# Kernel optimization log

Measured on AMD Instinct MI355X. Metric: run time of the kernel, lower is better.

Reference implementation:

```python
import jax, jax.numpy as jnp
import numpy as np

DECAY = 0.9


def setup_inputs() -> dict:
    key = jax.random.key(0)
    ks = jax.random.split(key, 8)
    B, L, d_model = 4, 2048, 1024
    d_state = 16
    d_inner = 2 * d_model  # expand=2
    x = jax.random.normal(ks[0], (B, L, d_model), dtype=jnp.float32)
    Win = jax.random.normal(ks[1], (d_model, d_inner), dtype=jnp.float32) / np.sqrt(d_model)
    bin_ = jnp.zeros((d_inner,), dtype=jnp.float32)
    Bp = jax.random.normal(ks[2], (d_inner, d_state), dtype=jnp.float32) * 0.01
    Cp = jax.random.normal(ks[3], (d_state, d_inner), dtype=jnp.float32) * 0.01
    Dp = jnp.ones((d_inner,), dtype=jnp.float32)
    Wout = jax.random.normal(ks[4], (d_inner, d_model), dtype=jnp.float32) / np.sqrt(d_inner)
    bout = jnp.zeros((d_model,), dtype=jnp.float32)
    return {"x": x, "Win": Win, "bin_": bin_, "Bp": Bp, "Cp": Cp, "Dp": Dp,
            "Wout": Wout, "bout": bout}


def reference(x, Win, bin_, Bp, Cp, Dp, Wout, bout):
    # x: [B, L, d_model]
    B, L, _ = x.shape
    d_inner, d_state = Bp.shape
    xi = jax.nn.silu(x @ Win + bin_)          # [B, L, d_inner]
    xt_seq = jnp.swapaxes(xi, 0, 1)            # [L, B, d_inner] for scan over time

    def step(h, xt):
        # h: [B, d_inner, d_state]; xt: [B, d_inner]
        h = h * DECAY + xt[:, :, None] * Bp[None, :, :]
        y = jnp.einsum('bij,ji->bi', h, Cp) + Dp * xt
        return h, y

    h0 = jnp.zeros((B, d_inner, d_state), dtype=x.dtype)
    _, ys = jax.lax.scan(step, h0, xt_seq)     # ys: [L, B, d_inner]
    y = jnp.swapaxes(ys, 0, 1)                 # [B, L, d_inner]
    return y @ Wout + bout                     # [B, L, d_model]
```

## Files before the change

kernel.cpp:

```cpp
#include <hip/hip_runtime.h>
#include <hip/hip_bf16.h>
#include <cstdint>
#include <cstddef>

typedef __attribute__((ext_vector_type(8))) short short8_t;
typedef __attribute__((ext_vector_type(4))) float f32x4;

__device__ __forceinline__ void gload16(const void* g, void* l) {
  __builtin_amdgcn_global_load_lds(
      (const __attribute__((address_space(1))) void*)g,
      (__attribute__((address_space(3))) void*)l, 16, 0, 0);
}

#define BARRIER() do { asm volatile("" ::: "memory"); __builtin_amdgcn_s_barrier(); asm volatile("" ::: "memory"); } while (0)
#define WVM6 asm volatile("s_waitcnt vmcnt(6)" ::: "memory")
#define WVM0 asm volatile("s_waitcnt vmcnt(0)" ::: "memory")
#define LGKM0 asm volatile("s_waitcnt lgkmcnt(0)" ::: "memory")

__global__ __launch_bounds__(256) void cvt_bf16_kernel(
    const float* __restrict__ in, __hip_bfloat16* __restrict__ out, int n) {
  int gid = blockIdx.x * blockDim.x + threadIdx.x;
  int idx = gid * 4;
  if (idx >= n) return;
  float4 v = *reinterpret_cast<const float4*>(in + idx);
  union { short4 s4; __hip_bfloat16 h[4]; } u;
  u.h[0] = __float2bfloat16(v.x);
  u.h[1] = __float2bfloat16(v.y);
  u.h[2] = __float2bfloat16(v.z);
  u.h[3] = __float2bfloat16(v.w);
  *reinterpret_cast<short4*>(out + idx) = u.s4;
}

__global__ __launch_bounds__(256) void transpose_cvt_kernel(
    const float* __restrict__ in, __hip_bfloat16* __restrict__ out, int R, int C) {
  __shared__ float tile[32][33];
  int c0 = blockIdx.x * 32, r0 = blockIdx.y * 32;
  int tx = threadIdx.x, ty = threadIdx.y;
#pragma unroll
  for (int j = 0; j < 32; j += 8)
    tile[ty + j][tx] = in[(size_t)(r0 + ty + j) * C + c0 + tx];
  __syncthreads();
#pragma unroll
  for (int j = 0; j < 32; j += 8)
    out[(size_t)(c0 + ty + j) * R + r0 + tx] = __float2bfloat16(tile[tx][ty + j]);
}

template <int EPI>
__global__ __launch_bounds__(512, 2) void gemm1b_kernel(
    const __hip_bfloat16* __restrict__ A,
    const __hip_bfloat16* __restrict__ Bt,
    const float* __restrict__ bias,
    void* __restrict__ Cout,
    int M, int N, int K) {
  constexpr int ABUF = 32768, BBUF = 16384;
  constexpr int BOFF = 3 * ABUF;
  __shared__ int4 ldsv[(3 * ABUF + 3 * BBUF) / 16];
  char* lds = (char*)ldsv;

  const int tid = threadIdx.x;
  const int l = tid & 63;
  const int w = tid >> 6;
  const int wm = w >> 1, wn = w & 1;
  const int fr = l & 15;
  const int sl = ((l >> 4) ^ ((fr >> 3) << 1)) * 16;
  const int arow_base = (wm * 64 + fr) * 64 + sl;
  const int brow_base = (wn * 64 + fr) * 64 + sl;

  const int nbn = N / 128;
  int bid = blockIdx.x;
  const int cpx = gridDim.x >> 3;
  bid = (bid & 7) * cpx + (bid >> 3);
  const int brow = (bid / nbn) * 256;
  const int bcol = (bid % nbn) * 128;
  const size_t K2 = (size_t)K * 2;

  int arA[2], acbA[2], dstA[2];
#pragma unroll
  for (int j = 0; j < 2; ++j) {
    int d = j * 8192 + w * 1024 + l * 16;
    int lg = d ^ (((d >> 9) & 1) << 5);
    arA[j] = lg >> 6;  acbA[j] = lg & 63;
    dstA[j] = j * 8192 + w * 1024;
  }
  int dB = w * 1024 + l * 16;
  int lgB = dB ^ (((dB >> 9) & 1) << 5);
  const int arB = lgB >> 6, acbB = lgB & 63, dstB = w * 1024;

  const char* Abp = (const char*)A;
  const char* Bbp = (const char*)Bt;

  auto stA = [&](int bufb, int kh, int tt) {
#pragma unroll
    for (int j = 0; j < 2; ++j)
      gload16(Abp + (size_t)(brow + arA[j]) * K2 + tt * 128 + kh * 64 + acbA[j],
              lds + bufb + kh * 16384 + dstA[j]);
  };
  auto stB = [&](int bufb, int kh, int tt) {
    gload16(Bbp + (size_t)(bcol + arB) * K2 + tt * 128 + kh * 64 + acbB,
            lds + BOFF + bufb + kh * 8192 + dstB);
  };

  f32x4 acc[4][4];
#pragma unroll
  for (int m = 0; m < 4; ++m)
#pragma unroll
    for (int n = 0; n < 4; ++n) acc[m][n] = (f32x4)0.f;

  const int NT = K >> 6;
  stA(0, 0, 0); stA(0, 1, 0); stB(0, 0, 0); stB(0, 1, 0);
  stA(ABUF, 0, 1); stA(ABUF, 1, 1); stB(BBUF, 0, 1); stB(BBUF, 1, 1);
  WVM6; BARRIER();

  int curA = 0, curB = 0, stAb = 2 * ABUF, stBb = 2 * BBUF;
  for (int T = 0; T < NT; ++T) {
    short8_t af[8], bf[8];
#pragma unroll
    for (int kh = 0; kh < 2; ++kh) {
#pragma unroll
      for (int mi = 0; mi < 4; ++mi)
        af[kh * 4 + mi] = *(const short8_t*)(lds + curA + kh * 16384 + arow_base + mi * 1024);
#pragma unroll
      for (int n = 0; n < 4; ++n)
        bf[kh * 4 + n] = *(const short8_t*)(lds + BOFF + curB + kh * 8192 + brow_base + n * 1024);
    }
    if (T + 2 < NT) {
      stA(stAb, 0, T + 2); stA(stAb, 1, T + 2);
      stB(stBb, 0, T + 2); stB(stBb, 1, T + 2);
    }
#pragma unroll
    for (int kh = 0; kh < 2; ++kh)
#pragma unroll
      for (int mi = 0; mi < 4; ++mi)
#pragma unroll
        for (int n = 0; n < 4; ++n)
          acc[mi][n] = __builtin_amdgcn_mfma_f32_16x16x32_bf16(
              af[kh * 4 + mi], bf[kh * 4 + n], acc[mi][n], 0, 0, 0);
    if (T + 1 < NT) {
      if (T + 2 < NT) { WVM6; } else { WVM0; }
      LGKM0;
      BARRIER();
    }
    curA += ABUF; if (curA == 3 * ABUF) curA = 0;
    curB += BBUF; if (curB == 3 * BBUF) curB = 0;
    stAb += ABUF; if (stAb == 3 * ABUF) stAb = 0;
    stBb += BBUF; if (stBb == 3 * BBUF) stBb = 0;
  }

  const int r0 = brow + wm * 64 + (l >> 4) * 4;
  const int c0 = bcol + wn * 64 + fr;
#pragma unroll
  for (int m = 0; m < 4; ++m) {
#pragma unroll
    for (int n = 0; n < 4; ++n) {
      const int col = c0 + n * 16;
      const float bv = bias[col];
#pragma unroll
      for (int j = 0; j < 4; ++j) {
        const int row = r0 + m * 16 + j;
        float v = acc[m][n][j] + bv;
        if constexpr (EPI == 0) {
          v = v / (1.0f + __expf(-v));
          ((__hip_bfloat16*)Cout)[(size_t)row * N + col] = __float2bfloat16(v);
        } else {
          ((float*)Cout)[(size_t)row * N + col] = v;
        }
      }
    }
  }
}

__global__ __launch_bounds__(256) void scan_kernel(
    const __hip_bfloat16* __restrict__ xi,
    const float* __restrict__ Bp,
    const float* __restrict__ Cp,
    const float* __restrict__ Dp,
    __hip_bfloat16* __restrict__ y) {
  constexpr int L = 2048, DI = 2048, DS = 16, TW = 256, H = 32;
  const int tid = threadIdx.x;
  const int bidx = blockIdx.x;
  const int iblk = bidx & 7;
  const int chunk = (bidx >> 3) & 7;
  const int b = bidx >> 6;
  const int i = iblk * 256 + tid;

  float cb = 0.f;
#pragma unroll
  for (int s = 0; s < DS; ++s) cb += Bp[i * DS + s] * Cp[s * DI + i];
  const float dp = Dp[i];

  const int t0 = chunk * TW;
  int tstart = t0 - H;
  if (tstart < 0) tstart = 0;

  const __hip_bfloat16* xp = xi + (size_t)(b * L) * DI + i;
  __hip_bfloat16* yp = y + (size_t)(b * L) * DI + i;

  float g = 0.f;
  const __hip_bfloat16* p = xp + (size_t)tstart * DI;
  for (int t = tstart; t < t0; ++t, p += DI)
    g = g * 0.9f + __bfloat162float(*p);
  __hip_bfloat16* q = yp + (size_t)t0 * DI;
  for (int t = 0; t < TW; ++t, p += DI, q += DI) {
    float xv = __bfloat162float(*p);
    g = g * 0.9f + xv;
    *q = __float2bfloat16(cb * g + dp * xv);
  }
}

extern "C" void kernel_launch(void* const* d_in, const int* in_sizes, int n_in,
                              void* d_out, int out_size, void* d_ws, size_t ws_size,
                              hipStream_t stream) {
  const float* x    = (const float*)d_in[0];
  const float* Win  = (const float*)d_in[1];
  const float* bin  = (const float*)d_in[2];
  const float* Bp   = (const float*)d_in[3];
  const float* Cp   = (const float*)d_in[4];
  const float* Dp   = (const float*)d_in[5];
  const float* Wout = (const float*)d_in[6];
  const float* bout = (const float*)d_in[7];
  float* out = (float*)d_out;

  constexpr int Bb = 4, L = 2048, DM = 1024, DI = 2048;
  constexpr int Mrows = Bb * L;

  char* ws = (char*)d_ws;
  __hip_bfloat16* xb    = (__hip_bfloat16*)ws;
  __hip_bfloat16* WinT  = (__hip_bfloat16*)(ws + (16u << 20));
  __hip_bfloat16* WoutT = (__hip_bfloat16*)(ws + (20u << 20));
  __hip_bfloat16* xi    = (__hip_bfloat16*)(ws + (24u << 20));
  __hip_bfloat16* yb    = (__hip_bfloat16*)(ws + (56u << 20));

  {
    int n = Mrows * DM;
    cvt_bf16_kernel<<<n / 1024, 256, 0, stream>>>(x, xb, n);
  }
  transpose_cvt_kernel<<<dim3(DI / 32, DM / 32), dim3(32, 8), 0, stream>>>(Win, WinT, DM, DI);
  transpose_cvt_kernel<<<dim3(DM / 32, DI / 32), dim3(32, 8), 0, stream>>>(Wout, WoutT, DI, DM);
  gemm1b_kernel<0><<<(Mrows / 256) * (DI / 128), 512, 0, stream>>>(
      xb, WinT, bin, (void*)xi, Mrows, DI, DM);
  scan_kernel<<<Bb * (L / 256) * (DI / 256), 256, 0, stream>>>(xi, Bp, Cp, Dp, yb);
  gemm1b_kernel<1><<<(Mrows / 256) * (DM / 128), 512, 0, stream>>>(
      yb, WoutT, bout, (void*)out, Mrows, DM, DI);
}
```

Baseline: 128.2 us.

## Shrink GEMM tiles to 128x128 with 256 threads and K-step 32

Replaces the 256x128-tile, 512-thread GEMM with a 128x128-tile, 256-thread kernel that processes 32-wide K slices per iteration through a 3-stage LDS ring. The prefetch for stage T+2 is issued before the LDS fragment reads rather than after. The aim is to cut LDS use so three blocks fit per CU and to produce more blocks for better CU balance. In exchange, each tile gets less data reuse and there are twice as many barriers per unit of K.

```diff
diff --git a/kernel.cpp b/kernel.cpp
--- a/kernel.cpp
+++ b/kernel.cpp
@@ -13,9 +13,8 @@
 }
 
 #define BARRIER() do { asm volatile("" ::: "memory"); __builtin_amdgcn_s_barrier(); asm volatile("" ::: "memory"); } while (0)
-#define WVM6 asm volatile("s_waitcnt vmcnt(6)" ::: "memory")
-#define WVM0 asm volatile("s_waitcnt vmcnt(0)" ::: "memory")
 #define LGKM0 asm volatile("s_waitcnt lgkmcnt(0)" ::: "memory")
+#define WVM(n) asm volatile("s_waitcnt vmcnt(" #n ")" ::: "memory")
 
 __global__ __launch_bounds__(256) void cvt_bf16_kernel(
     const float* __restrict__ in, __hip_bfloat16* __restrict__ out, int n) {
@@ -46,15 +45,15 @@
 }
 
 template <int EPI>
-__global__ __launch_bounds__(512, 2) void gemm1b_kernel(
+__global__ __launch_bounds__(256, 3) void gemm_cr_kernel(
     const __hip_bfloat16* __restrict__ A,
     const __hip_bfloat16* __restrict__ Bt,
     const float* __restrict__ bias,
     void* __restrict__ Cout,
     int M, int N, int K) {
-  constexpr int ABUF = 32768, BBUF = 16384;
-  constexpr int BOFF = 3 * ABUF;
-  __shared__ int4 ldsv[(3 * ABUF + 3 * BBUF) / 16];
+  constexpr int AUNIT = 8192, BUNIT = 8192;
+  constexpr int BOFF = 3 * AUNIT;
+  __shared__ int4 ldsv[(3 * AUNIT + 3 * BUNIT) / 16];
   char* lds = (char*)ldsv;
 
   const int tid = threadIdx.x;
@@ -63,42 +62,39 @@
   const int wm = w >> 1, wn = w & 1;
   const int fr = l & 15;
   const int sl = ((l >> 4) ^ ((fr >> 3) << 1)) * 16;
-  const int arow_base = (wm * 64 + fr) * 64 + sl;
-  const int brow_base = (wn * 64 + fr) * 64 + sl;
+  const int arowb = (wm * 64 + fr) * 64 + sl;
+  const int browb = (wn * 64 + fr) * 64 + sl;
 
   const int nbn = N / 128;
   int bid = blockIdx.x;
   const int cpx = gridDim.x >> 3;
   bid = (bid & 7) * cpx + (bid >> 3);
-  const int brow = (bid / nbn) * 256;
+  const int brow = (bid / nbn) * 128;
   const int bcol = (bid % nbn) * 128;
   const size_t K2 = (size_t)K * 2;
 
-  int arA[2], acbA[2], dstA[2];
+  int ar[2], acb[2], dst[2];
 #pragma unroll
   for (int j = 0; j < 2; ++j) {
-    int d = j * 8192 + w * 1024 + l * 16;
+    int d = j * 4096 + tid * 16;
     int lg = d ^ (((d >> 9) & 1) << 5);
-    arA[j] = lg >> 6;  acbA[j] = lg & 63;
-    dstA[j] = j * 8192 + w * 1024;
-  }
-  int dB = w * 1024 + l * 16;
-  int lgB = dB ^ (((dB >> 9) & 1) << 5);
-  const int arB = lgB >> 6, acbB = lgB & 63, dstB = w * 1024;
+    ar[j] = lg >> 6;  acb[j] = lg & 63;
+    dst[j] = j * 4096 + w * 1024;
+  }
 
   const char* Abp = (const char*)A;
   const char* Bbp = (const char*)Bt;
 
-  auto stA = [&](int bufb, int kh, int tt) {
+  auto stAB = [&](int t, int buf) {
+    const int ab = buf * AUNIT;
 #pragma unroll
     for (int j = 0; j < 2; ++j)
-      gload16(Abp + (size_t)(brow + arA[j]) * K2 + tt * 128 + kh * 64 + acbA[j],
-              lds + bufb + kh * 16384 + dstA[j]);
+      gload16(Abp + (size_t)(brow + ar[j]) * K2 + t * 64 + acb[j], lds + ab + dst[j]);
+    const int bb = BOFF + buf * BUNIT;
+#pragma unroll
+    for (int j = 0; j < 2; ++j)
+      gload16(Bbp + (size_t)(bcol + ar[j]) * K2 + t * 64 + acb[j], lds + bb + dst[j]);
   };
-  auto stB = [&](int bufb, int kh, int tt) {
-    gload16(Bbp + (size_t)(bcol + arB) * K2 + tt * 128 + kh * 64 + acbB,
-            lds + BOFF + bufb + kh * 8192 + dstB);
-  };
 
   f32x4 acc[4][4];
 #pragma unroll
@@ -106,44 +102,33 @@
 #pragma unroll
     for (int n = 0; n < 4; ++n) acc[m][n] = (f32x4)0.f;
 
-  const int NT = K >> 6;
-  stA(0, 0, 0); stA(0, 1, 0); stB(0, 0, 0); stB(0, 1, 0);
-  stA(ABUF, 0, 1); stA(ABUF, 1, 1); stB(BBUF, 0, 1); stB(BBUF, 1, 1);
-  WVM6; BARRIER();
-
-  int curA = 0, curB = 0, stAb = 2 * ABUF, stBb = 2 * BBUF;
+  const int NT = K >> 5;
+  stAB(0, 0); stAB(1, 1);
+  WVM(4); BARRIER();
+
+  int cur = 0, stg = 2;
   for (int T = 0; T < NT; ++T) {
-    short8_t af[8], bf[8];
-#pragma unroll
-    for (int kh = 0; kh < 2; ++kh) {
-#pragma unroll
-      for (int mi = 0; mi < 4; ++mi)
-        af[kh * 4 + mi] = *(const short8_t*)(lds + curA + kh * 16384 + arow_base + mi * 1024);
+    if (T + 2 < NT) stAB(T + 2, stg);
+    short8_t af[4], bf[4];
+    const int ab = cur * AUNIT, bb = BOFF + cur * BUNIT;
+#pragma unroll
+    for (int mi = 0; mi < 4; ++mi)
+      af[mi] = *(const short8_t*)(lds + ab + arowb + mi * 1024);
+#pragma unroll
+    for (int n = 0; n < 4; ++n)
+      bf[n] = *(const short8_t*)(lds + bb + browb + n * 1024);
+#pragma unroll
+    for (int mi = 0; mi < 4; ++mi)
 #pragma unroll
       for (int n = 0; n < 4; ++n)
-        bf[kh * 4 + n] = *(const short8_t*)(lds + BOFF + curB + kh * 8192 + brow_base + n * 1024);
-    }
-    if (T + 2 < NT) {
-      stA(stAb, 0, T + 2); stA(stAb, 1, T + 2);
-      stB(stBb, 0, T + 2); stB(stBb, 1, T + 2);
-    }
-#pragma unroll
-    for (int kh = 0; kh < 2; ++kh)
-#pragma unroll
-      for (int mi = 0; mi < 4; ++mi)
-#pragma unroll
-        for (int n = 0; n < 4; ++n)
-          acc[mi][n] = __builtin_amdgcn_mfma_f32_16x16x32_bf16(
-              af[kh * 4 + mi], bf[kh * 4 + n], acc[mi][n], 0, 0, 0);
+        acc[mi][n] = __builtin_amdgcn_mfma_f32_16x16x32_bf16(af[mi], bf[n], acc[mi][n], 0, 0, 0);
     if (T + 1 < NT) {
-      if (T + 2 < NT) { WVM6; } else { WVM0; }
+      if (T + 2 < NT) { WVM(4); } else { WVM(0); }
       LGKM0;
       BARRIER();
     }
-    curA += ABUF; if (curA == 3 * ABUF) curA = 0;
-    curB += BBUF; if (curB == 3 * BBUF) curB = 0;
-    stAb += ABUF; if (stAb == 3 * ABUF) stAb = 0;
-    stBb += BBUF; if (stBb == 3 * BBUF) stBb = 0;
+    cur = (cur == 2) ? 0 : cur + 1;
+    stg = (stg == 2) ? 0 : stg + 1;
   }
 
   const int r0 = brow + wm * 64 + (l >> 4) * 4;
@@ -236,9 +221,9 @@
   }
   transpose_cvt_kernel<<<dim3(DI / 32, DM / 32), dim3(32, 8), 0, stream>>>(Win, WinT, DM, DI);
   transpose_cvt_kernel<<<dim3(DM / 32, DI / 32), dim3(32, 8), 0, stream>>>(Wout, WoutT, DI, DM);
-  gemm1b_kernel<0><<<(Mrows / 256) * (DI / 128), 512, 0, stream>>>(
+  gemm_cr_kernel<0><<<(Mrows / 128) * (DI / 128), 256, 0, stream>>>(
       xb, WinT, bin, (void*)xi, Mrows, DI, DM);
   scan_kernel<<<Bb * (L / 256) * (DI / 256), 256, 0, stream>>>(xi, Bp, Cp, Dp, yb);
-  gemm1b_kernel<1><<<(Mrows / 256) * (DM / 128), 512, 0, stream>>>(
+  gemm_cr_kernel<1><<<(Mrows / 128) * (DM / 128), 256, 0, stream>>>(
       yb, WoutT, bout, (void*)out, Mrows, DM, DI);
 }
```

Result: slower. 133.0 us (+3.8%).

## Use 4-wave 256x128 GEMM with larger per-wave tiles for input projection

Applied to the files above, without the earlier changes.

Adds a dedicated kernel for the first GEMM. It uses 256 threads (4 waves), so each wave computes a 128x64 output tile with 32 accumulators, and steps K in chunks of 32 with a 3-stage LDS pipeline. It also raises wave priority around the MFMA block with s_setprio. The intent is more MFMA work per LDS fragment load and less synchronisation overhead per tile, at the cost of higher register pressure and fewer waves per block. The second GEMM is simplified to a non-templated float-output version.

```diff
diff --git a/kernel.cpp b/kernel.cpp
--- a/kernel.cpp
+++ b/kernel.cpp
@@ -13,9 +13,8 @@
 }
 
 #define BARRIER() do { asm volatile("" ::: "memory"); __builtin_amdgcn_s_barrier(); asm volatile("" ::: "memory"); } while (0)
-#define WVM6 asm volatile("s_waitcnt vmcnt(6)" ::: "memory")
-#define WVM0 asm volatile("s_waitcnt vmcnt(0)" ::: "memory")
 #define LGKM0 asm volatile("s_waitcnt lgkmcnt(0)" ::: "memory")
+#define WVM(n) asm volatile("s_waitcnt vmcnt(" #n ")" ::: "memory")
 
 __global__ __launch_bounds__(256) void cvt_bf16_kernel(
     const float* __restrict__ in, __hip_bfloat16* __restrict__ out, int n) {
@@ -45,12 +44,117 @@
     out[(size_t)(c0 + ty + j) * R + r0 + tx] = __float2bfloat16(tile[tx][ty + j]);
 }
 
-template <int EPI>
+__global__ __launch_bounds__(256, 2) void gemm_bm256_kernel(
+    const __hip_bfloat16* __restrict__ A,
+    const __hip_bfloat16* __restrict__ Bt,
+    const float* __restrict__ bias,
+    __hip_bfloat16* __restrict__ Cout,
+    int M, int N, int K) {
+  constexpr int AUNIT = 16384, BUNIT = 8192;
+  constexpr int BOFF = 3 * AUNIT;
+  __shared__ int4 ldsv[(3 * AUNIT + 3 * BUNIT) / 16];
+  char* lds = (char*)ldsv;
+
+  const int tid = threadIdx.x;
+  const int l = tid & 63;
+  const int w = tid >> 6;
+  const int wm = w >> 1, wn = w & 1;
+  const int fr = l & 15;
+  const int sl = ((l >> 4) ^ ((fr >> 3) << 1)) * 16;
+  const int arowb = (wm * 128 + fr) * 64 + sl;
+  const int browb = (wn * 64 + fr) * 64 + sl;
+
+  const int nbn = N / 128;
+  int bid = blockIdx.x;
+  const int cpx = gridDim.x >> 3;
+  bid = (bid & 7) * cpx + (bid >> 3);
+  const int brow = (bid / nbn) * 256;
+  const int bcol = (bid % nbn) * 128;
+  const size_t K2 = (size_t)K * 2;
+
+  int ar[4], acb[4], dst[4];
+#pragma unroll
+  for (int j = 0; j < 4; ++j) {
+    int d = j * 4096 + tid * 16;
+    int lg = d ^ (((d >> 9) & 1) << 5);
+    ar[j] = lg >> 6;  acb[j] = lg & 63;
+    dst[j] = j * 4096 + w * 1024;
+  }
+
+  const char* Abp = (const char*)A;
+  const char* Bbp = (const char*)Bt;
+
+  auto stAB = [&](int t, int buf) {
+#pragma unroll
+    for (int j = 0; j < 4; ++j)
+      gload16(Abp + (size_t)(brow + ar[j]) * K2 + (size_t)t * 64 + acb[j],
+              lds + buf * AUNIT + dst[j]);
+#pragma unroll
+    for (int j = 0; j < 2; ++j)
+      gload16(Bbp + (size_t)(bcol + ar[j]) * K2 + (size_t)t * 64 + acb[j],
+              lds + BOFF + buf * BUNIT + dst[j]);
+  };
+
+  f32x4 acc[8][4];
+#pragma unroll
+  for (int m = 0; m < 8; ++m)
+#pragma unroll
+    for (int n = 0; n < 4; ++n) acc[m][n] = (f32x4)0.f;
+
+  const int NT = K >> 5;
+  stAB(0, 0); stAB(1, 1);
+  WVM(6); BARRIER();
+
+  int cur = 0, stg = 2;
+  for (int T = 0; T < NT; ++T) {
+    if (T + 2 < NT) stAB(T + 2, stg);
+    short8_t af[8], bf[4];
+#pragma unroll
+    for (int mi = 0; mi < 8; ++mi)
+      af[mi] = *(const short8_t*)(lds + cur * AUNIT + arowb + mi * 1024);
+#pragma unroll
+    for (int n = 0; n < 4; ++n)
+      bf[n] = *(const short8_t*)(lds + BOFF + cur * BUNIT + browb + n * 1024);
+    __builtin_amdgcn_s_setprio(1);
+#pragma unroll
+    for (int mi = 0; mi < 8; ++mi)
+#pragma unroll
+      for (int n = 0; n < 4; ++n)
+        acc[mi][n] = __builtin_amdgcn_mfma_f32_16x16x32_bf16(af[mi], bf[n], acc[mi][n], 0, 0, 0);
+    __builtin_amdgcn_s_setprio(0);
+    if (T + 1 < NT) {
+      if (T + 2 < NT) { WVM(6); } else { WVM(0); }
+      LGKM0;
+      BARRIER();
+    }
+    cur = (cur == 2) ? 0 : cur + 1;
+    stg = (stg == 2) ? 0 : stg + 1;
+  }
+
+  const int r0 = brow + wm * 128 + (l >> 4) * 4;
+  const int c0 = bcol + wn * 64 + fr;
+#pragma unroll
+  for (int m = 0; m < 8; ++m) {
+#pragma unroll
+    for (int n = 0; n < 4; ++n) {
+      const int col = c0 + n * 16;
+      const float bv = bias[col];
+#pragma unroll
+      for (int j = 0; j < 4; ++j) {
+        const int row = r0 + m * 16 + j;
+        float v = acc[m][n][j] + bv;
+        v = v / (1.0f + __expf(-v));
+        Cout[(size_t)row * N + col] = __float2bfloat16(v);
+      }
+    }
+  }
+}
+
 __global__ __launch_bounds__(512, 2) void gemm1b_kernel(
     const __hip_bfloat16* __restrict__ A,
     const __hip_bfloat16* __restrict__ Bt,
     const float* __restrict__ bias,
-    void* __restrict__ Cout,
+    float* __restrict__ Cout,
     int M, int N, int K) {
   constexpr int ABUF = 32768, BBUF = 16384;
   constexpr int BOFF = 3 * ABUF;
@@ -109,7 +213,7 @@
   const int NT = K >> 6;
   stA(0, 0, 0); stA(0, 1, 0); stB(0, 0, 0); stB(0, 1, 0);
   stA(ABUF, 0, 1); stA(ABUF, 1, 1); stB(BBUF, 0, 1); stB(BBUF, 1, 1);
-  WVM6; BARRIER();
+  WVM(6); BARRIER();
 
   int curA = 0, curB = 0, stAb = 2 * ABUF, stBb = 2 * BBUF;
   for (int T = 0; T < NT; ++T) {
@@ -136,7 +240,7 @@
           acc[mi][n] = __builtin_amdgcn_mfma_f32_16x16x32_bf16(
               af[kh * 4 + mi], bf[kh * 4 + n], acc[mi][n], 0, 0, 0);
     if (T + 1 < NT) {
-      if (T + 2 < NT) { WVM6; } else { WVM0; }
+      if (T + 2 < NT) { WVM(6); } else { WVM(0); }
       LGKM0;
       BARRIER();
     }
@@ -157,13 +261,7 @@
 #pragma unroll
       for (int j = 0; j < 4; ++j) {
         const int row = r0 + m * 16 + j;
-        float v = acc[m][n][j] + bv;
-        if constexpr (EPI == 0) {
-          v = v / (1.0f + __expf(-v));
-          ((__hip_bfloat16*)Cout)[(size_t)row * N + col] = __float2bfloat16(v);
-        } else {
-          ((float*)Cout)[(size_t)row * N + col] = v;
-        }
+        Cout[(size_t)row * N + col] = acc[m][n][j] + bv;
       }
     }
   }
@@ -236,9 +334,9 @@
   }
   transpose_cvt_kernel<<<dim3(DI / 32, DM / 32), dim3(32, 8), 0, stream>>>(Win, WinT, DM, DI);
   transpose_cvt_kernel<<<dim3(DM / 32, DI / 32), dim3(32, 8), 0, stream>>>(Wout, WoutT, DI, DM);
-  gemm1b_kernel<0><<<(Mrows / 256) * (DI / 128), 512, 0, stream>>>(
-      xb, WinT, bin, (void*)xi, Mrows, DI, DM);
+  gemm_bm256_kernel<<<(Mrows / 256) * (DI / 128), 256, 0, stream>>>(
+      xb, WinT, bin, xi, Mrows, DI, DM);
   scan_kernel<<<Bb * (L / 256) * (DI / 256), 256, 0, stream>>>(xi, Bp, Cp, Dp, yb);
-  gemm1b_kernel<1><<<(Mrows / 256) * (DM / 128), 512, 0, stream>>>(
-      yb, WoutT, bout, (void*)out, Mrows, DM, DI);
-}
+  gemm1b_kernel<<<(Mrows / 256) * (DM / 128), 512, 0, stream>>>(
+      yb, WoutT, bout, out, Mrows, DM, DI);
+}
```

Result: faster. 123.4 us (-3.8%).
